# Kernel tuning notes

Hardware: AMD Instinct MI355X
Metric: run time of the kernel (lower is better)

The kernel has to match this reference:

```python
import jax, jax.numpy as jnp
import numpy as np

B, L, D_MODEL, D_INNER, P = 4, 16384, 256, 512, 64  # P = d_state, conj_sym=False
STEP_RESCALE = 1.0


def setup_inputs() -> dict:
    key = jax.random.key(0)
    ks = jax.random.split(key, 11)
    # projections (bias=False)
    W_in = jax.random.normal(ks[0], (D_MODEL, 2 * D_INNER), jnp.float32) * (1.0 / np.sqrt(D_MODEL))
    W_out = jax.random.normal(ks[1], (D_INNER, D_MODEL), jnp.float32) * (1.0 / np.sqrt(D_INNER))
    # diagonal SSM params: Lambda = A_real + i*A_imag, HiPPO-like (negative real part)
    A_real = -0.5 * jnp.ones((P,), jnp.float32) - jax.random.uniform(ks[2], (P,), jnp.float32)
    A_imag = jnp.pi * jnp.arange(P, dtype=jnp.float32) * (jax.random.uniform(ks[3], (P,), jnp.float32) * 0.1 + 0.95)
    B_re = jax.random.normal(ks[4], (P, D_INNER), jnp.float32) * (1.0 / np.sqrt(P))
    B_im = jax.random.normal(ks[5], (P, D_INNER), jnp.float32) * (1.0 / np.sqrt(P))
    C_re = jax.random.normal(ks[6], (D_INNER, P), jnp.float32) * (1.0 / np.sqrt(D_INNER))
    C_im = jax.random.normal(ks[7], (D_INNER, P), jnp.float32) * (1.0 / np.sqrt(D_INNER))
    D = jax.random.normal(ks[8], (D_INNER,), jnp.float32)
    # dt ~ loguniform[dt_min, dt_max]; inv_dt = softplus^{-1}(dt) = dt + log(-expm1(-dt))
    dt = jnp.exp(jax.random.uniform(ks[9], (P,), jnp.float32) * (np.log(0.1) - np.log(0.001)) + np.log(0.001))
    dt = jnp.clip(dt, 1e-4, None)
    inv_dt = dt + jnp.log(-jnp.expm1(-dt))
    x = jax.random.normal(ks[10], (B, L, D_MODEL), jnp.float32)
    return {"x": x, "W_in": W_in, "W_out": W_out, "A_real": A_real, "A_imag": A_imag,
            "B_re": B_re, "B_im": B_im, "C_re": C_re, "C_im": C_im, "D": D, "inv_dt": inv_dt}


def _binop(e1, e2):
    a1, b1 = e1
    a2, b2 = e2
    return a2 * a1, a2 * b1 + b2


def reference(x, W_in, W_out, A_real, A_imag, B_re, B_im, C_re, C_im, D, inv_dt):
    # in_proj + gate split
    x_and_res = x @ W_in                       # (b, l, 2*d_inner)
    u, res = jnp.split(x_and_res, 2, axis=-1)
    u = jax.nn.silu(u)                         # (b, l, d_inner)
    # bilinear discretization of diagonal SSM
    A = A_real + 1j * A_imag                   # (P,)
    dt = STEP_RESCALE * jax.nn.softplus(inv_dt)  # (P,)
    BL = 1.0 / (1.0 - (dt / 2.0) * A)
    dA = BL * (1.0 + (dt / 2.0) * A)           # (P,)
    dB = (BL * dt)[:, None] * (B_re + 1j * B_im)  # (P, d_inner)
    # drive: Bu_t = dB @ u_t
    Bu = u.astype(dA.dtype) @ dB.T             # (b, l, P) complex
    # parallel (associative) scan of h_t = dA*h_{t-1} + Bu_t  (h_0 = 0)
    elems = (jnp.broadcast_to(dA, Bu.shape), Bu)
    _, h = jax.lax.associative_scan(_binop, elems, axis=1)  # (b, l, P)
    C = C_re + 1j * C_im                       # (d_inner, P)
    y = jnp.real(h @ C.T) + D * u              # (b, l, d_inner), + skip D*u
    y = y * jax.nn.silu(res)
    return y @ W_out                           # (b, l, d_model)
```

## Files before the change

### kernel.cpp

```cpp
#include <hip/hip_runtime.h>
#include <math.h>

#define NTOK 65536
#define LSEQ 16384
#define GCH 64
#define NCH 256

typedef __attribute__((ext_vector_type(8))) short short8v;
typedef __attribute__((ext_vector_type(4))) float f32x4;
typedef unsigned short u16;

__device__ __forceinline__ u16 f2bf(float f) {
  unsigned u = __float_as_uint(f);
  return (u16)((u + 0x7FFFu + ((u >> 16) & 1u)) >> 16);
}
__device__ __forceinline__ float bf2f(u16 b) {
  return __uint_as_float(((unsigned)b) << 16);
}
__device__ __forceinline__ unsigned cvtpk_bf16(float lo, float hi) {
  unsigned r;
  asm("v_cvt_pk_bf16_f32 %0, %1, %2" : "=v"(r) : "v"(lo), "v"(hi));
  return r;
}
__device__ __forceinline__ float silu_f(float v) {
  return v * __builtin_amdgcn_rcpf(1.f + __expf(-v));
}
__device__ __forceinline__ void gld16(const u16* g, u16* l) {
  __builtin_amdgcn_global_load_lds((const __attribute__((address_space(1))) void*)g,
                                   (__attribute__((address_space(3))) void*)l, 16, 0, 0);
}

#define WAITV2 asm volatile("s_waitcnt vmcnt(2) lgkmcnt(0)" ::: "memory")
#define WAITV1 asm volatile("s_waitcnt vmcnt(1) lgkmcnt(0)" ::: "memory")
#define WAITV0 asm volatile("s_waitcnt vmcnt(0) lgkmcnt(0)" ::: "memory")
#define BARRAW asm volatile("s_barrier" ::: "memory")

__global__ void setup_scalar_k(const float* __restrict__ A_real, const float* __restrict__ A_imag,
                               const float* __restrict__ inv_dt,
                               float2* __restrict__ dAf, float2* __restrict__ fvec,
                               float2* __restrict__ powt) {
  int p = threadIdx.x;
  if (p >= 64) return;
  double ar = (double)A_real[p], ai = (double)A_imag[p];
  double dt = log1p(exp((double)inv_dt[p]));
  double zr = 0.5 * dt * ar, zi = 0.5 * dt * ai;
  double d1r = 1.0 - zr;
  double den = d1r * d1r + zi * zi;
  double blr = d1r / den, bli = zi / den;
  double nr = 1.0 + zr, ni = zi;
  double dar = blr * nr - bli * ni;
  double dai = blr * ni + bli * nr;
  dAf[p] = make_float2((float)dar, (float)dai);
  fvec[p] = make_float2((float)(blr * dt), (float)(bli * dt));
  double cr = 1.0, ci = 0.0;
  for (int k = 0; k <= GCH; ++k) {
    powt[p * (GCH + 1) + k] = make_float2((float)cr, (float)ci);
    double t = cr * dar - ci * dai;
    ci = cr * dai + ci * dar;
    cr = t;
  }
}

__global__ void setup_tables_k(const float* __restrict__ B_re, const float* __restrict__ B_im,
                               const float* __restrict__ C_re, const float* __restrict__ C_im,
                               const float* __restrict__ W_in, const float* __restrict__ W_out,
                               const float2* __restrict__ fvec,
                               u16* __restrict__ WinT, u16* __restrict__ dBn,
                               u16* __restrict__ Ccb, u16* __restrict__ WoutT) {
  int idx = blockIdx.x * blockDim.x + threadIdx.x;
  int stride = gridDim.x * blockDim.x;
  for (int i = idx; i < 1024 * 256; i += stride) {
    int n = i >> 8, k = i & 255;
    WinT[i] = f2bf(W_in[k * 1024 + n]);
  }
  for (int i = idx; i < 128 * 512; i += stride) {
    int p = i >> 9, d = i & 511;
    float2 f = fvec[p & 63];
    float br = B_re[(p & 63) * 512 + d], bi = B_im[(p & 63) * 512 + d];
    float v = (p < 64) ? (f.x * br - f.y * bi) : (f.x * bi + f.y * br);
    dBn[i] = f2bf(v);
  }
  for (int i = idx; i < 512 * 128; i += stride) {
    int d = i >> 7, k = i & 127;
    float v = (k < 64) ? C_re[d * 64 + k] : -C_im[d * 64 + (k - 64)];
    Ccb[i] = f2bf(v);
  }
  for (int i = idx; i < 256 * 512; i += stride) {
    int n = i >> 9, k = i & 511;
    WoutT[i] = f2bf(W_out[k * 256 + n]);
  }
}

__global__ __launch_bounds__(256) void cvt_x_k(const float* __restrict__ x, u16* __restrict__ xb) {
  size_t i = ((size_t)blockIdx.x * blockDim.x + threadIdx.x) * 4;
  size_t stride = (size_t)gridDim.x * blockDim.x * 4;
  const size_t total = (size_t)NTOK * 256;
  for (; i < total; i += stride) {
    float4 v = *(const float4*)(x + i);
    ushort4 o;
    o.x = f2bf(v.x); o.y = f2bf(v.y); o.z = f2bf(v.z); o.w = f2bf(v.w);
    *(ushort4*)(xb + i) = o;
  }
}

__global__ __launch_bounds__(512) void k1_gemm(
    const u16* __restrict__ A, const u16* __restrict__ Bt,
    u16* __restrict__ u_bf, u16* __restrict__ sr_bf) {
  constexpr int KDIM = 256, NT = 8;
  __shared__ u16 As[3][128 * 32];
  __shared__ u16 Bs[3][128 * 32];
  const int tid = threadIdx.x;
  const int w = tid >> 6, l = tid & 63;
  const int wm = w >> 2, wn = w & 3;

  const int lin = blockIdx.x;
  const int cpx = gridDim.x >> 3;
  const int swz = (lin & 7) * cpx + (lin >> 3);
  const int n0 = (swz & 7) * 128;
  const int m0 = (swz >> 3) * 128;

  f32x4 acc[4][2] = {};

  const int lr = l >> 2;
  const int sc = (l & 3) ^ ((l >> 3) & 3);
  const u16* gA = A + (size_t)(m0 + w * 16 + lr) * KDIM + sc * 8;
  const u16* gB = Bt + (size_t)(n0 + w * 16 + lr) * KDIM + sc * 8;

  const int fr = l & 15;
  const int kgs = (((l >> 4) ^ (l >> 1)) & 3) * 8;

  auto stage = [&](int buf, int k0) {
    gld16(gA + k0, &As[buf][w * 512]);
    gld16(gB + k0, &Bs[buf][w * 512]);
  };
  auto compute = [&](int buf) {
    short8v af[4], bfr[2];
#pragma unroll
    for (int mi = 0; mi < 4; ++mi)
      af[mi] = *(const short8v*)&As[buf][(wm * 64 + mi * 16 + fr) * 32 + kgs];
#pragma unroll
    for (int ni = 0; ni < 2; ++ni)
      bfr[ni] = *(const short8v*)&Bs[buf][(wn * 32 + ni * 16 + fr) * 32 + kgs];
#pragma unroll
    for (int mi = 0; mi < 4; ++mi)
#pragma unroll
      for (int ni = 0; ni < 2; ++ni)
        acc[mi][ni] = __builtin_amdgcn_mfma_f32_16x16x32_bf16(af[mi], bfr[ni], acc[mi][ni], 0, 0, 0);
  };

  stage(0, 0);
  stage(1, 32);
#pragma unroll
  for (int t = 0; t < NT; ++t) {
    if (t + 1 < NT) { WAITV2; } else { WAITV0; }
    BARRAW;
    if (t + 2 < NT) stage((t + 2) % 3, (t + 2) * 32);
    compute(t % 3);
  }

  const int rbase = (l >> 4) * 4;
  u16* Cw = (n0 < 512) ? u_bf : sr_bf;
  const int cb = (n0 < 512) ? n0 : (n0 - 512);
#pragma unroll
  for (int mi = 0; mi < 4; ++mi) {
#pragma unroll
    for (int ni = 0; ni < 2; ++ni) {
      int gr0 = m0 + wm * 64 + mi * 16 + rbase;
      int col = cb + wn * 32 + ni * 16 + fr;
      float s0 = silu_f(acc[mi][ni][0]);
      float s1 = silu_f(acc[mi][ni][1]);
      float s2 = silu_f(acc[mi][ni][2]);
      float s3 = silu_f(acc[mi][ni][3]);
      unsigned p01 = cvtpk_bf16(s0, s1);
      unsigned p23 = cvtpk_bf16(s2, s3);
      Cw[(size_t)(gr0 + 0) * 512 + col] = (u16)p01;
      Cw[(size_t)(gr0 + 1) * 512 + col] = (u16)(p01 >> 16);
      Cw[(size_t)(gr0 + 2) * 512 + col] = (u16)p23;
      Cw[(size_t)(gr0 + 3) * 512 + col] = (u16)(p23 >> 16);
    }
  }
}

template<int MODE, int LOG_NBX, int KDIM>
__global__ __launch_bounds__(1024) void mgemm2(
    const u16* __restrict__ Ain, const u16* __restrict__ Bt,
    void* __restrict__ C0, void* __restrict__ C1,
    const float* __restrict__ Dvec) {
  constexpr int NT = KDIM / 32;
  __shared__ u16 As[3][128 * 32];
  __shared__ u16 Bs[3][256 * 32];
  const int tid = threadIdx.x;
  const int w = tid >> 6, l = tid & 63;
  const int wm = w >> 3, wn = w & 7;
  const bool isA = (w < 8);

  const int lin = blockIdx.x;
  const int cpx = gridDim.x >> 3;
  const int swz = (lin & 7) * cpx + (lin >> 3);
  const int n0 = (swz & ((1 << LOG_NBX) - 1)) * 256;
  const int m0 = (swz >> LOG_NBX) * 128;

  f32x4 acc[4][2] = {};

  const int fr = l & 15;
  const int kgs = (((l >> 4) ^ (l >> 1)) & 3) * 8;
  const int sr = l >> 2;
  const int scs = (l & 3) ^ ((l >> 3) & 3);

  const u16* gA = nullptr;
  const u16* gB = nullptr;
  if (isA) gA = Ain + (size_t)(m0 + w * 16 + sr) * KDIM + scs * 8;
  else     gB = Bt + (size_t)(n0 + (w - 8) * 16 + sr) * KDIM + scs * 8;

  auto stage = [&](int buf, int k0) {
    if (isA) {
      gld16(gA + k0, &As[buf][w * 512]);
    } else {
      gld16(gB + k0, &Bs[buf][(w - 8) * 512]);
      gld16(gB + k0 + (size_t)128 * KDIM, &Bs[buf][(w - 8) * 512 + 4096]);
    }
  };
  auto compute = [&](int buf) {
    short8v af[4], bfr[2];
#pragma unroll
    for (int mi = 0; mi < 4; ++mi)
      af[mi] = *(const short8v*)&As[buf][(wm * 64 + mi * 16 + fr) * 32 + kgs];
#pragma unroll
    for (int ni = 0; ni < 2; ++ni)
      bfr[ni] = *(const short8v*)&Bs[buf][(wn * 32 + ni * 16 + fr) * 32 + kgs];
#pragma unroll
    for (int mi = 0; mi < 4; ++mi)
#pragma unroll
      for (int ni = 0; ni < 2; ++ni)
        acc[mi][ni] = __builtin_amdgcn_mfma_f32_16x16x32_bf16(af[mi], bfr[ni], acc[mi][ni], 0, 0, 0);
  };

  stage(0, 0);
  stage(1, 32);
#pragma unroll
  for (int t = 0; t < NT; ++t) {
    if (t + 1 < NT) { if (isA) { WAITV1; } else { WAITV2; } } else { WAITV0; }
    BARRAW;
    if (t + 2 < NT) stage((t + 2) % 3, (t + 2) * 32);
    compute(t % 3);
  }

  const int rbase = (l >> 4) * 4;
#pragma unroll
  for (int mi = 0; mi < 4; ++mi) {
#pragma unroll
    for (int ni = 0; ni < 2; ++ni) {
      int gr0 = m0 + wm * 64 + mi * 16 + rbase;
      int gc = n0 + wn * 32 + ni * 16 + fr;
      if (MODE == 2) {
        float g[4];
#pragma unroll
        for (int j = 0; j < 4; ++j) {
          size_t r = (size_t)(gr0 + j);
          float uu = bf2f(((const u16*)C0)[r * 512 + gc]);
          float sr2 = bf2f(((const u16*)C1)[r * 512 + gc]);
          g[j] = (acc[mi][ni][j] + Dvec[gc] * uu) * sr2;
        }
        unsigned p01 = cvtpk_bf16(g[0], g[1]);
        unsigned p23 = cvtpk_bf16(g[2], g[3]);
        ((u16*)C1)[(size_t)(gr0 + 0) * 512 + gc] = (u16)p01;
        ((u16*)C1)[(size_t)(gr0 + 1) * 512 + gc] = (u16)(p01 >> 16);
        ((u16*)C1)[(size_t)(gr0 + 2) * 512 + gc] = (u16)p23;
        ((u16*)C1)[(size_t)(gr0 + 3) * 512 + gc] = (u16)(p23 >> 16);
      } else {
#pragma unroll
        for (int j = 0; j < 4; ++j)
          ((float*)C0)[(size_t)(gr0 + j) * 256 + gc] = acc[mi][ni][j];
      }
    }
  }
}

__global__ __launch_bounds__(512) void k2_bu_carry(
    const u16* __restrict__ A, const u16* __restrict__ Bt,
    float* __restrict__ Bu, float* __restrict__ carr, float* __restrict__ carr2,
    const float2* __restrict__ dAf, const float2* __restrict__ powt) {
  constexpr int KDIM = 512;
  constexpr int NT = KDIM / 32;
  __shared__ u16 As[3][128 * 32];
  __shared__ u16 Bs[3][128 * 32];
  const int tid = threadIdx.x;
  const int w = tid >> 6, l = tid & 63;
  const int wm = w >> 2, wn = w & 3;

  const int lin = blockIdx.x;
  const int cpx = gridDim.x >> 3;
  const int swz = (lin & 7) * cpx + (lin >> 3);
  const int m0 = swz * 128;

  f32x4 acc[4][2] = {};

  const int lr = l >> 2;
  const int sc = (l & 3) ^ ((l >> 3) & 3);
  const u16* gA = A + (size_t)(m0 + w * 16 + lr) * KDIM + sc * 8;
  const u16* gB = Bt + (size_t)(w * 16 + lr) * KDIM + sc * 8;

  const int fr = l & 15;
  const int kgs = (((l >> 4) ^ (l >> 1)) & 3) * 8;

  auto stage = [&](int buf, int k0) {
    gld16(gA + k0, &As[buf][w * 512]);
    gld16(gB + k0, &Bs[buf][w * 512]);
  };
  auto compute = [&](int buf) {
    short8v af[4], bfr[2];
#pragma unroll
    for (int mi = 0; mi < 4; ++mi)
      af[mi] = *(const short8v*)&As[buf][(wm * 64 + mi * 16 + fr) * 32 + kgs];
#pragma unroll
    for (int ni = 0; ni < 2; ++ni)
      bfr[ni] = *(const short8v*)&Bs[buf][(wn * 32 + ni * 16 + fr) * 32 + kgs];
#pragma unroll
    for (int mi = 0; mi < 4; ++mi)
#pragma unroll
      for (int ni = 0; ni < 2; ++ni)
        acc[mi][ni] = __builtin_amdgcn_mfma_f32_16x16x32_bf16(af[mi], bfr[ni], acc[mi][ni], 0, 0, 0);
  };

  stage(0, 0);
  stage(1, 32);
#pragma unroll
  for (int t = 0; t < NT; ++t) {
    if (t + 1 < NT) { WAITV2; } else { WAITV0; }
    BARRAW;
    if (t + 2 < NT) stage((t + 2) % 3, (t + 2) * 32);
    compute(t % 3);
  }

  const int lg = l >> 4;
  const int rbase = lg * 4;
#pragma unroll
  for (int mi = 0; mi < 4; ++mi)
#pragma unroll
    for (int ni = 0; ni < 2; ++ni) {
      int gr0 = m0 + wm * 64 + mi * 16 + rbase;
      int gc = wn * 32 + ni * 16 + fr;
#pragma unroll
      for (int j = 0; j < 4; ++j)
        Bu[(size_t)(gr0 + j) * 128 + gc] = acc[mi][ni][j];
    }
  const int cu = (m0 >> 6) + wm;
#pragma unroll
  for (int ni = 0; ni < 2; ++ni) {
    int gc = wn * 32 + ni * 16 + fr;
    int p = gc & 63;
    float2 dA = dAf[p];
    float sre = 0.f, sim = 0.f;
#pragma unroll
    for (int mi = 0; mi < 4; ++mi) {
      float tr = 0.f, ti = 0.f;
#pragma unroll
      for (int j = 0; j < 4; ++j) {
        float v = acc[mi][ni][j];
        float nr = fmaf(dA.x, tr, fmaf(-dA.y, ti, v));
        float nim = fmaf(dA.x, ti, dA.y * tr);
        tr = nr; ti = nim;
      }
      float2 wg = powt[p * (GCH + 1) + 60 - lg * 4 - 16 * mi];
      sre = fmaf(wg.x, tr, fmaf(-wg.y, ti, sre));
      sim = fmaf(wg.x, ti, fmaf(wg.y, tr, sim));
    }
    sre += __shfl_xor(sre, 16); sim += __shfl_xor(sim, 16);
    sre += __shfl_xor(sre, 32); sim += __shfl_xor(sim, 32);
    if (lg == 0) {
      size_t crow = (size_t)cu * 128;
      if (gc < 64) { carr[crow + p] = sre;  carr[crow + 64 + p] = sim; }
      else         { carr2[crow + p] = -sim; carr2[crow + 64 + p] = sre; }
    }
  }
}

__global__ void scan_carry_k(const float* __restrict__ carr, const float* __restrict__ carr2,
                             float* __restrict__ offc, const float2* __restrict__ powt) {
  int b = threadIdx.x >> 6;
  int p = threadIdx.x & 63;
  float2 dAG = powt[p * (GCH + 1) + GCH];
  float rr = 0.f, ri = 0.f;
  float a0[8], b0[8], c0a[8], d0a[8];
  float a1[8], b1[8], c1a[8], d1a[8];

#define LOADB(cb, A_, B_, C_, D_)                                      \
  {                                                                     \
    _Pragma("unroll") for (int j = 0; j < 8; ++j) {                     \
      size_t crow = (size_t)(b * NCH + (cb) + j) * 128;                 \
      A_[j] = carr[crow + p]; B_[j] = carr[crow + 64 + p];              \
      C_[j] = carr2[crow + p]; D_[j] = carr2[crow + 64 + p];            \
    }                                                                   \
  }
#define STEPB(cb, A_, B_, C_, D_)                                      \
  {                                                                     \
    _Pragma("unroll") for (int j = 0; j < 8; ++j) {                     \
      size_t orow = (size_t)(b * NCH + (cb) + j) * 128;                 \
      offc[orow + p] = rr; offc[orow + 64 + p] = ri;                    \
      float er = A_[j] + C_[j], ei = B_[j] + D_[j];                     \
      float nr = fmaf(dAG.x, rr, fmaf(-dAG.y, ri, er));                 \
      float ni = fmaf(dAG.x, ri, fmaf(dAG.y, rr, ei));                  \
      rr = nr; ri = ni;                                                 \
    }                                                                   \
  }

  LOADB(0, a0, b0, c0a, d0a);
  for (int c0 = 0; c0 < NCH; c0 += 16) {
    LOADB(c0 + 8, a1, b1, c1a, d1a);
    STEPB(c0, a0, b0, c0a, d0a);
    if (c0 + 16 < NCH) LOADB(c0 + 16, a0, b0, c0a, d0a);
    STEPB(c0 + 8, a1, b1, c1a, d1a);
  }
#undef LOADB
#undef STEPB
}

__global__ __launch_bounds__(256) void scan_emit_k(const float* __restrict__ Bu,
                                                   const float* __restrict__ offc,
                                                   u16* __restrict__ hb,
                                                   const float2* __restrict__ dAf) {
  int unit = blockIdx.x * 4 + (threadIdx.x >> 6);
  int p = threadIdx.x & 63;
  int b = unit >> 8, c = unit & 255;
  float2 dA = dAf[p];
  size_t base = ((size_t)b * LSEQ + (size_t)c * GCH) * 128;
  float hr = offc[(size_t)unit * 128 + p];
  float hi = offc[(size_t)unit * 128 + 64 + p];
  for (int i0 = 0; i0 < GCH; i0 += 8) {
    float br[8], bi[8];
#pragma unroll
    for (int j = 0; j < 8; ++j) {
      br[j] = Bu[base + (size_t)(i0 + j) * 128 + p];
      bi[j] = Bu[base + (size_t)(i0 + j) * 128 + 64 + p];
    }
#pragma unroll
    for (int j = 0; j < 8; ++j) {
      float nr = fmaf(dA.x, hr, fmaf(-dA.y, hi, br[j]));
      float ni = fmaf(dA.x, hi, fmaf(dA.y, hr, bi[j]));
      hr = nr; hi = ni;
      hb[base + (size_t)(i0 + j) * 128 + p] = f2bf(hr);
      hb[base + (size_t)(i0 + j) * 128 + 64 + p] = f2bf(hi);
    }
  }
}

extern "C" void kernel_launch(void* const* d_in, const int* in_sizes, int n_in,
                              void* d_out, int out_size, void* d_ws, size_t ws_size,
                              hipStream_t stream) {
  const float* x      = (const float*)d_in[0];
  const float* W_in   = (const float*)d_in[1];
  const float* W_out  = (const float*)d_in[2];
  const float* A_real = (const float*)d_in[3];
  const float* A_imag = (const float*)d_in[4];
  const float* B_re   = (const float*)d_in[5];
  const float* B_im   = (const float*)d_in[6];
  const float* C_re   = (const float*)d_in[7];
  const float* C_im   = (const float*)d_in[8];
  const float* Dv     = (const float*)d_in[9];
  const float* inv_dt = (const float*)d_in[10];

  u16* xb    = (u16*)d_ws;
  u16* u_bf  = xb + (size_t)NTOK * 256;
  u16* sr_bf = u_bf + (size_t)NTOK * 512;
  u16* h_bf  = sr_bf + (size_t)NTOK * 512;
  u16* WinT  = h_bf + (size_t)NTOK * 128;
  u16* dBn   = WinT + 1024 * 256;
  u16* Ccb   = dBn + 128 * 512;
  u16* WoutT = Ccb + 512 * 128;

  float* O    = (float*)d_out;
  float* Bu   = O;
  float* offc = O + 8388608;
  float* carr = O + 8519680;
  float* car2 = O + 8650752;
  float2* powt = (float2*)(O + 8781824);
  float2* dAf  = (float2*)(O + 8790144);
  float2* fvec = (float2*)(O + 8790272);

  setup_scalar_k<<<1, 64, 0, stream>>>(A_real, A_imag, inv_dt, dAf, fvec, powt);
  setup_tables_k<<<256, 256, 0, stream>>>(B_re, B_im, C_re, C_im, W_in, W_out, fvec,
                                          WinT, dBn, Ccb, WoutT);
  cvt_x_k<<<2048, 256, 0, stream>>>(x, xb);

  k1_gemm<<<4096, 512, 0, stream>>>(xb, WinT, u_bf, sr_bf);
  k2_bu_carry<<<512, 512, 0, stream>>>(u_bf, dBn, Bu, carr, car2, dAf, powt);
  scan_carry_k<<<1, 256, 0, stream>>>(carr, car2, offc, powt);
  scan_emit_k<<<256, 256, 0, stream>>>(Bu, offc, h_bf, dAf);
  mgemm2<2, 1, 128><<<1024, 1024, 0, stream>>>(h_bf, Ccb, u_bf, sr_bf, Dv);
  mgemm2<3, 0, 512><<<512, 1024, 0, stream>>>(sr_bf, WoutT, O, nullptr, nullptr);
}
```

Measured before the change: 210.6 us.

## Unify GEMMs into 512-thread 128x256 tile kernel with 64x64 per-wave tiles

Replaces the 1024-thread mgemm2 (8 waves loading A, 8 loading B, 32x64 per wave) and the separate 128x128 k1_gemm with one 512-thread kernel. In it every wave loads both A and B slices and computes a 64x64 sub-tile with 4x4 MFMA accumulators. The in_proj GEMM now uses 128x256 tiles with the SiLU epilogue folded in as MODE 0. The goal is more MFMA work per LDS fragment load and fewer blocks for in_proj. The cost is higher register pressure from doubling the accumulators, with launch bounds set to allow 4 blocks per CU.

Result: slower. 232.6 us (+10.4%).

```diff
diff --git a/kernel.cpp b/kernel.cpp
--- a/kernel.cpp
+++ b/kernel.cpp
@@ -30,8 +30,8 @@
                                    (__attribute__((address_space(3))) void*)l, 16, 0, 0);
 }
 
+#define WAITV3 asm volatile("s_waitcnt vmcnt(3) lgkmcnt(0)" ::: "memory")
 #define WAITV2 asm volatile("s_waitcnt vmcnt(2) lgkmcnt(0)" ::: "memory")
-#define WAITV1 asm volatile("s_waitcnt vmcnt(1) lgkmcnt(0)" ::: "memory")
 #define WAITV0 asm volatile("s_waitcnt vmcnt(0) lgkmcnt(0)" ::: "memory")
 #define BARRAW asm volatile("s_barrier" ::: "memory")
 
@@ -103,86 +103,8 @@
   }
 }
 
-__global__ __launch_bounds__(512) void k1_gemm(
-    const u16* __restrict__ A, const u16* __restrict__ Bt,
-    u16* __restrict__ u_bf, u16* __restrict__ sr_bf) {
-  constexpr int KDIM = 256, NT = 8;
-  __shared__ u16 As[3][128 * 32];
-  __shared__ u16 Bs[3][128 * 32];
-  const int tid = threadIdx.x;
-  const int w = tid >> 6, l = tid & 63;
-  const int wm = w >> 2, wn = w & 3;
-
-  const int lin = blockIdx.x;
-  const int cpx = gridDim.x >> 3;
-  const int swz = (lin & 7) * cpx + (lin >> 3);
-  const int n0 = (swz & 7) * 128;
-  const int m0 = (swz >> 3) * 128;
-
-  f32x4 acc[4][2] = {};
-
-  const int lr = l >> 2;
-  const int sc = (l & 3) ^ ((l >> 3) & 3);
-  const u16* gA = A + (size_t)(m0 + w * 16 + lr) * KDIM + sc * 8;
-  const u16* gB = Bt + (size_t)(n0 + w * 16 + lr) * KDIM + sc * 8;
-
-  const int fr = l & 15;
-  const int kgs = (((l >> 4) ^ (l >> 1)) & 3) * 8;
-
-  auto stage = [&](int buf, int k0) {
-    gld16(gA + k0, &As[buf][w * 512]);
-    gld16(gB + k0, &Bs[buf][w * 512]);
-  };
-  auto compute = [&](int buf) {
-    short8v af[4], bfr[2];
-#pragma unroll
-    for (int mi = 0; mi < 4; ++mi)
-      af[mi] = *(const short8v*)&As[buf][(wm * 64 + mi * 16 + fr) * 32 + kgs];
-#pragma unroll
-    for (int ni = 0; ni < 2; ++ni)
-      bfr[ni] = *(const short8v*)&Bs[buf][(wn * 32 + ni * 16 + fr) * 32 + kgs];
-#pragma unroll
-    for (int mi = 0; mi < 4; ++mi)
-#pragma unroll
-      for (int ni = 0; ni < 2; ++ni)
-        acc[mi][ni] = __builtin_amdgcn_mfma_f32_16x16x32_bf16(af[mi], bfr[ni], acc[mi][ni], 0, 0, 0);
-  };
-
-  stage(0, 0);
-  stage(1, 32);
-#pragma unroll
-  for (int t = 0; t < NT; ++t) {
-    if (t + 1 < NT) { WAITV2; } else { WAITV0; }
-    BARRAW;
-    if (t + 2 < NT) stage((t + 2) % 3, (t + 2) * 32);
-    compute(t % 3);
-  }
-
-  const int rbase = (l >> 4) * 4;
-  u16* Cw = (n0 < 512) ? u_bf : sr_bf;
-  const int cb = (n0 < 512) ? n0 : (n0 - 512);
-#pragma unroll
-  for (int mi = 0; mi < 4; ++mi) {
-#pragma unroll
-    for (int ni = 0; ni < 2; ++ni) {
-      int gr0 = m0 + wm * 64 + mi * 16 + rbase;
-      int col = cb + wn * 32 + ni * 16 + fr;
-      float s0 = silu_f(acc[mi][ni][0]);
-      float s1 = silu_f(acc[mi][ni][1]);
-      float s2 = silu_f(acc[mi][ni][2]);
-      float s3 = silu_f(acc[mi][ni][3]);
-      unsigned p01 = cvtpk_bf16(s0, s1);
-      unsigned p23 = cvtpk_bf16(s2, s3);
-      Cw[(size_t)(gr0 + 0) * 512 + col] = (u16)p01;
-      Cw[(size_t)(gr0 + 1) * 512 + col] = (u16)(p01 >> 16);
-      Cw[(size_t)(gr0 + 2) * 512 + col] = (u16)p23;
-      Cw[(size_t)(gr0 + 3) * 512 + col] = (u16)(p23 >> 16);
-    }
-  }
-}
-
 template<int MODE, int LOG_NBX, int KDIM>
-__global__ __launch_bounds__(1024) void mgemm2(
+__global__ __launch_bounds__(512, 4) void mgemm3(
     const u16* __restrict__ Ain, const u16* __restrict__ Bt,
     void* __restrict__ C0, void* __restrict__ C1,
     const float* __restrict__ Dvec) {
@@ -191,8 +113,7 @@
   __shared__ u16 Bs[3][256 * 32];
   const int tid = threadIdx.x;
   const int w = tid >> 6, l = tid & 63;
-  const int wm = w >> 3, wn = w & 7;
-  const bool isA = (w < 8);
+  const int wm = w >> 2, wn = w & 3;
 
   const int lin = blockIdx.x;
   const int cpx = gridDim.x >> 3;
@@ -200,38 +121,33 @@
   const int n0 = (swz & ((1 << LOG_NBX) - 1)) * 256;
   const int m0 = (swz >> LOG_NBX) * 128;
 
-  f32x4 acc[4][2] = {};
+  f32x4 acc[4][4] = {};
 
   const int fr = l & 15;
   const int kgs = (((l >> 4) ^ (l >> 1)) & 3) * 8;
-  const int sr = l >> 2;
+  const int lr = l >> 2;
   const int scs = (l & 3) ^ ((l >> 3) & 3);
 
-  const u16* gA = nullptr;
-  const u16* gB = nullptr;
-  if (isA) gA = Ain + (size_t)(m0 + w * 16 + sr) * KDIM + scs * 8;
-  else     gB = Bt + (size_t)(n0 + (w - 8) * 16 + sr) * KDIM + scs * 8;
+  const u16* gA = Ain + (size_t)(m0 + w * 16 + lr) * KDIM + scs * 8;
+  const u16* gB = Bt + (size_t)(n0 + w * 16 + lr) * KDIM + scs * 8;
 
   auto stage = [&](int buf, int k0) {
-    if (isA) {
-      gld16(gA + k0, &As[buf][w * 512]);
-    } else {
-      gld16(gB + k0, &Bs[buf][(w - 8) * 512]);
-      gld16(gB + k0 + (size_t)128 * KDIM, &Bs[buf][(w - 8) * 512 + 4096]);
-    }
+    gld16(gA + k0, &As[buf][w * 512]);
+    gld16(gB + k0, &Bs[buf][w * 512]);
+    gld16(gB + k0 + (size_t)128 * KDIM, &Bs[buf][4096 + w * 512]);
   };
   auto compute = [&](int buf) {
-    short8v af[4], bfr[2];
+    short8v af[4], bfr[4];
 #pragma unroll
     for (int mi = 0; mi < 4; ++mi)
       af[mi] = *(const short8v*)&As[buf][(wm * 64 + mi * 16 + fr) * 32 + kgs];
 #pragma unroll
-    for (int ni = 0; ni < 2; ++ni)
-      bfr[ni] = *(const short8v*)&Bs[buf][(wn * 32 + ni * 16 + fr) * 32 + kgs];
+    for (int ni = 0; ni < 4; ++ni)
+      bfr[ni] = *(const short8v*)&Bs[buf][(wn * 64 + ni * 16 + fr) * 32 + kgs];
 #pragma unroll
     for (int mi = 0; mi < 4; ++mi)
 #pragma unroll
-      for (int ni = 0; ni < 2; ++ni)
+      for (int ni = 0; ni < 4; ++ni)
         acc[mi][ni] = __builtin_amdgcn_mfma_f32_16x16x32_bf16(af[mi], bfr[ni], acc[mi][ni], 0, 0, 0);
   };
 
@@ -239,7 +155,7 @@
   stage(1, 32);
 #pragma unroll
   for (int t = 0; t < NT; ++t) {
-    if (t + 1 < NT) { if (isA) { WAITV1; } else { WAITV2; } } else { WAITV0; }
+    if (t + 1 < NT) { WAITV3; } else { WAITV0; }
     BARRAW;
     if (t + 2 < NT) stage((t + 2) % 3, (t + 2) * 32);
     compute(t % 3);
@@ -249,10 +165,23 @@
 #pragma unroll
   for (int mi = 0; mi < 4; ++mi) {
 #pragma unroll
-    for (int ni = 0; ni < 2; ++ni) {
+    for (int ni = 0; ni < 4; ++ni) {
       int gr0 = m0 + wm * 64 + mi * 16 + rbase;
-      int gc = n0 + wn * 32 + ni * 16 + fr;
-      if (MODE == 2) {
+      int gc = n0 + wn * 64 + ni * 16 + fr;
+      if (MODE == 0) {
+        float s0 = silu_f(acc[mi][ni][0]);
+        float s1 = silu_f(acc[mi][ni][1]);
+        float s2 = silu_f(acc[mi][ni][2]);
+        float s3 = silu_f(acc[mi][ni][3]);
+        unsigned p01 = cvtpk_bf16(s0, s1);
+        unsigned p23 = cvtpk_bf16(s2, s3);
+        u16* Cw = (n0 < 512) ? (u16*)C0 : (u16*)C1;
+        int col = gc - ((n0 < 512) ? 0 : 512);
+        Cw[(size_t)(gr0 + 0) * 512 + col] = (u16)p01;
+        Cw[(size_t)(gr0 + 1) * 512 + col] = (u16)(p01 >> 16);
+        Cw[(size_t)(gr0 + 2) * 512 + col] = (u16)p23;
+        Cw[(size_t)(gr0 + 3) * 512 + col] = (u16)(p23 >> 16);
+      } else if (MODE == 2) {
         float g[4];
 #pragma unroll
         for (int j = 0; j < 4; ++j) {
@@ -482,10 +411,10 @@
                                           WinT, dBn, Ccb, WoutT);
   cvt_x_k<<<2048, 256, 0, stream>>>(x, xb);
 
-  k1_gemm<<<4096, 512, 0, stream>>>(xb, WinT, u_bf, sr_bf);
+  mgemm3<0, 2, 256><<<2048, 512, 0, stream>>>(xb, WinT, u_bf, sr_bf, nullptr);
   k2_bu_carry<<<512, 512, 0, stream>>>(u_bf, dBn, Bu, carr, car2, dAf, powt);
   scan_carry_k<<<1, 256, 0, stream>>>(carr, car2, offc, powt);
   scan_emit_k<<<256, 256, 0, stream>>>(Bu, offc, h_bf, dAf);
-  mgemm2<2, 1, 128><<<1024, 1024, 0, stream>>>(h_bf, Ccb, u_bf, sr_bf, Dv);
-  mgemm2<3, 0, 512><<<512, 1024, 0, stream>>>(sr_bf, WoutT, O, nullptr, nullptr);
-}
+  mgemm3<2, 1, 128><<<1024, 512, 0, stream>>>(h_bf, Ccb, u_bf, sr_bf, Dv);
+  mgemm3<3, 0, 512><<<512, 512, 0, stream>>>(sr_bf, WoutT, O, nullptr, nullptr);
+}
```
